# Kernel optimization log

Hardware: AMD Instinct MI355X
Metric: run time of the kernel (lower is better)

Reference implementation:

```python
import jax, jax.numpy as jnp
import numpy as np

BS, SEQ, D_IN, D_OUT = 4, 1024, 1024, 1024
N_SKILLS, RANK = 8, 4
SCALING = 1.0  # lora_alpha / rank, folded into one constant
NEG_INF = -1e38


def setup_inputs() -> dict:
    key = jax.random.key(0)
    ks = jax.random.split(key, 5)
    x = jax.random.normal(ks[0], (BS, SEQ, D_IN), jnp.float32)
    phi = jax.random.normal(ks[1], (D_IN, N_SKILLS), jnp.float32) * 0.02
    lora_a = jax.random.normal(ks[2], (N_SKILLS, D_IN, RANK), jnp.float32) * 0.02
    lora_b = jax.random.normal(ks[3], (N_SKILLS, RANK, D_OUT), jnp.float32) * 0.02
    W = jax.random.normal(ks[4], (D_OUT, D_IN), jnp.float32) * 0.02
    b = jnp.zeros((D_OUT,), jnp.float32)
    # left-padded sequences with an instruction prefix right after the padding
    pad_len = np.array([100, 0, 250, 50])
    inst_len = 300
    pad = np.zeros((BS, SEQ), np.int32)
    inst = np.zeros((BS, SEQ), np.int32)
    for i in range(BS):
        pad[i, pad_len[i]:] = 1
        inst[i, pad_len[i]:pad_len[i] + inst_len] = 1
    return {"x": x, "phi": phi, "lora_a": lora_a, "lora_b": lora_b,
            "W": W, "b": b,
            "inst_mask": jnp.asarray(inst), "pad_mask": jnp.asarray(pad)}


def _causal_prefix_mask(inst_mask, pad_mask):
    # faithful port of create_causal_prefix_mask (padding_side='left')
    bs, seq = inst_mask.shape
    first_one = jnp.argmax(inst_mask, axis=1, keepdims=True)          # [b,1]
    n_ones = jnp.sum(inst_mask, axis=1, keepdims=True)                # [b,1]
    thresh = first_one + n_ones                                       # last_one_idx + 1
    exp = jnp.broadcast_to(thresh, (bs, seq))                         # [b,s]
    inv = jnp.maximum(seq - exp - jnp.arange(seq)[None, :], 0)[:, ::-1]
    m = (exp + inv) * pad_mask                                        # [b,s]
    m3 = m[:, :, None] * pad_mask[:, None, :]                         # [b,s,s]
    ar = jnp.arange(seq)[None, None, :]
    return ar < m3                                                    # bool [b,s,s]


def reference(x, phi, lora_a, lora_b, W, b, inst_mask, pad_mask):
    # router: mixing logits per token per skill
    mw = jnp.einsum('bsd,dn->bsn', x, phi)                            # [b,s,k]
    cm = _causal_prefix_mask(inst_mask, pad_mask)                     # [b,s,s]
    padf = pad_mask.astype(x.dtype)
    # expand over attended positions p, mask, softmax over p
    logits = jnp.where(cm[..., None], mw[:, :, None, :], NEG_INF)     # [b,s,p,k]
    logits = jnp.transpose(logits, (0, 3, 1, 2))                      # [b,k,s,p]
    D = jax.nn.softmax(logits, axis=-1)
    D = D * padf[:, None, :, None]                                    # zero padded query rows
    # token mixing: contract over source tokens (last axis of D)
    input_mixed = jnp.einsum('bsd,bkps->bkpd', x, D)                  # [b,k,s,d]
    # per-skill LoRA (n_splits == 1, q squeezed)
    ar_r = jnp.einsum('bksd,kdr->bskr', input_mixed, lora_a)          # [b,s,k,r]
    ad = jnp.einsum('bskr,krd->bskd', ar_r, lora_b)                   # [b,s,k,d_out]
    # softmax-weighted combine over skills
    C = jax.nn.softmax(mw, axis=-1)
    adapter_out = jnp.einsum('bsk,bskd->bsd', C, ad) * SCALING
    base = jnp.einsum('bsd,od->bso', x, W) + b
    return base + adapter_out
```

## Files before the change

kernel.cpp:

```cpp
#include <hip/hip_runtime.h>
#include <hip/hip_bf16.h>
#include <cstdint>

#define SEQ   1024
#define DOUT  1024
#define KDIM  1024
#define MTOT  4096
#define WCROWS 1104

typedef __bf16 bf16x8 __attribute__((ext_vector_type(8)));
typedef float  f32x4  __attribute__((ext_vector_type(4)));

__device__ inline unsigned short f2bf(float f) {
  union { float f; unsigned u; } a; a.f = f;
  unsigned r = a.u + 0x7fff + ((a.u >> 16) & 1);
  return (unsigned short)(r >> 16);
}

__device__ inline void gl16(const void* g, void* l) {
  __builtin_amdgcn_global_load_lds((__attribute__((address_space(1))) void*)g,
                                   (__attribute__((address_space(3))) void*)l, 16, 0, 0);
}

__global__ __launch_bounds__(256) void k_prep(const float4* __restrict__ x, ushort4* __restrict__ xb,
                                              const float* __restrict__ W, const float* __restrict__ phi,
                                              const float* __restrict__ la, const float* __restrict__ lb,
                                              unsigned short* __restrict__ Wc,
                                              const int* __restrict__ inst, int* __restrict__ thr) {
  int blk = blockIdx.x, tid = threadIdx.x;
  if (blk < 4096) {
    int i = blk * 256 + tid;
    float4 v = x[i];
    ushort4 o; o.x = f2bf(v.x); o.y = f2bf(v.y); o.z = f2bf(v.z); o.w = f2bf(v.w);
    xb[i] = o;
  } else if (blk < 8512) {
    int i = (blk - 4096) * 256 + tid;
    int row = i >> 10, d = i & 1023;
    float v;
    if (row < 1024)       v = W[i];
    else if (row < 1032)  v = phi[d * 8 + (row - 1024)];
    else if (row < 1064)  { int kr = row - 1032; v = la[(kr >> 2) * 4096 + d * 4 + (kr & 3)]; }
    else if (row < 1072)  v = 0.f;
    else                  v = lb[(row - 1072) * 1024 + d];
    Wc[i] = f2bf(v);
  } else {
    int b = tid >> 6, lane = tid & 63;
    int fo = 1 << 30, no = 0;
#pragma unroll
    for (int j = 0; j < 16; ++j) {
      int p = j * 64 + lane;
      int iv = inst[b * SEQ + p];
      if (iv > 0) fo = min(fo, p);
      no += iv;
    }
#pragma unroll
    for (int d = 1; d < 64; d <<= 1) { fo = min(fo, __shfl_xor(fo, d)); no += __shfl_xor(no, d); }
    if (lane == 0) thr[b] = (no > 0) ? fo + no : 0;
  }
}

__global__ __launch_bounds__(256) void k_mwz(const unsigned short* __restrict__ xb,
                                             const unsigned short* __restrict__ Wc,
                                             float* __restrict__ mwzP) {
  __shared__ unsigned short As[64 * 32];
  __shared__ unsigned short Bs[48 * 32];
  int bm = blockIdx.x, ks = blockIdx.y;
  int t = threadIdx.x, wave = t >> 6, lane = t & 63;
  int quad = lane >> 4, lr = lane & 15;
  f32x4 acc[3];
#pragma unroll
  for (int i = 0; i < 3; ++i) acc[i] = (f32x4){0.f, 0.f, 0.f, 0.f};
  const unsigned short* aG = xb + (size_t)bm * 64 * KDIM + ks * 256;
  const unsigned short* bG = Wc + (size_t)1024 * KDIM + ks * 256;
  int r0 = t >> 2, c0 = (t & 3) * 8;
  for (int kb = 0; kb < 256; kb += 32) {
    __syncthreads();
    gl16(aG + (size_t)r0 * KDIM + kb + c0, &As[wave * 512]);
    if (t < 192) gl16(bG + (size_t)r0 * KDIM + kb + c0, &Bs[wave * 512]);
    __syncthreads();
    bf16x8 af = *(const bf16x8*)&As[(wave * 16 + lr) * 32 + quad * 8];
#pragma unroll
    for (int ni = 0; ni < 3; ++ni) {
      bf16x8 bfr = *(const bf16x8*)&Bs[(ni * 16 + lr) * 32 + quad * 8];
      acc[ni] = __builtin_amdgcn_mfma_f32_16x16x32_bf16(af, bfr, acc[ni], 0, 0, 0);
    }
  }
#pragma unroll
  for (int ni = 0; ni < 3; ++ni) {
    int c = ni * 16 + lr;
#pragma unroll
    for (int rg = 0; rg < 4; ++rg) {
      int row = bm * 64 + wave * 16 + quad * 4 + rg;
      if (c < 40) mwzP[(size_t)(ks * 40 + c) * MTOT + row] = acc[ni][rg];
    }
  }
}

__global__ __launch_bounds__(1024) void k_scan_gate(const float* __restrict__ mwzP,
                                                    const int* __restrict__ pad, const int* __restrict__ thr,
                                                    unsigned short* __restrict__ gb) {
  int b = blockIdx.x, c = blockIdx.y;
  int tid = threadIdx.x, wv = tid >> 6, lane = tid & 63;
  __shared__ float wsz[16], wsp[16];
  __shared__ float sv, spc;
  int q = b * SEQ + tid;
  float pm = (float)pad[q];
  float z = 0.f;
#pragma unroll
  for (int s = 0; s < 4; ++s) z += mwzP[(size_t)(s * 40 + 8 + c) * MTOT + q];
  z *= pm;
  float vz = z, vp = pm;
#pragma unroll
  for (int d = 1; d < 64; d <<= 1) {
    float oz = __shfl_up(vz, d), op = __shfl_up(vp, d);
    if (lane >= d) { vz += oz; vp += op; }
  }
  if (lane == 63) { wsz[wv] = vz; wsp[wv] = vp; }
  __syncthreads();
  if (wv == 0 && lane < 16) {
    float oz = wsz[lane], op = wsp[lane], sz = oz, sp = op;
#pragma unroll
    for (int d = 1; d < 16; d <<= 1) {
      float tz = __shfl_up(sz, d), tp = __shfl_up(sp, d);
      if (lane >= d) { sz += tz; sp += tp; }
    }
    wsz[lane] = sz - oz; wsp[lane] = sp - op;
  }
  __syncthreads();
  vz += wsz[wv]; vp += wsp[wv];
  int th = thr[b];
  if (th > 0 && tid == th - 1) { sv = vz; spc = vp; }
  __syncthreads();
  unsigned short o = 0;
  if (pm != 0.f) {
    bool own = (tid + 1 >= th);
    float Tv  = own ? vz : sv;
    float cnt = own ? vp : spc;
    float C[8], mx = -1e30f;
#pragma unroll
    for (int k = 0; k < 8; ++k) {
      float m = 0.f;
#pragma unroll
      for (int s = 0; s < 4; ++s) m += mwzP[(size_t)(s * 40 + k) * MTOT + q];
      C[k] = m; mx = fmaxf(mx, m);
    }
    float sm = 0.f;
#pragma unroll
    for (int k = 0; k < 8; ++k) { C[k] = __expf(C[k] - mx); sm += C[k]; }
    o = f2bf(C[c >> 2] * Tv / (sm * cnt));
  }
  gb[(size_t)q * 32 + c] = o;
}

__global__ __launch_bounds__(256) void k_gemm(const unsigned short* __restrict__ A,
                                              const unsigned short* __restrict__ Wc,
                                              const unsigned short* __restrict__ gb,
                                              float* __restrict__ out,
                                              const float* __restrict__ bias) {
  __shared__ unsigned short As[128 * 32];
  __shared__ unsigned short Bs[64 * 32];
  int bm = blockIdx.x, bn = blockIdx.y;
  int t = threadIdx.x;
  int wave = t >> 6, lane = t & 63;
  int wr = wave >> 1, wc = wave & 1;
  int quad = lane >> 4, lr = lane & 15;
  f32x4 acc[4][2];
#pragma unroll
  for (int i = 0; i < 4; i++)
#pragma unroll
    for (int j = 0; j < 2; j++) acc[i][j] = (f32x4){0.f, 0.f, 0.f, 0.f};

  const unsigned short* aG = A + (size_t)bm * 128 * KDIM;
  const unsigned short* bG = Wc + (size_t)bn * 64 * KDIM;
  int r0 = t >> 2, c0 = (t & 3) * 8;

  for (int kb = 0; kb < KDIM; kb += 32) {
    __syncthreads();
    gl16(aG + (size_t)r0 * KDIM + kb + c0, &As[wave * 512]);
    gl16(aG + (size_t)(r0 + 64) * KDIM + kb + c0, &As[2048 + wave * 512]);
    gl16(bG + (size_t)r0 * KDIM + kb + c0, &Bs[wave * 512]);
    __syncthreads();
    bf16x8 af[4], bfr[2];
#pragma unroll
    for (int mi = 0; mi < 4; mi++) af[mi]  = *(const bf16x8*)&As[(wr * 64 + mi * 16 + lr) * 32 + quad * 8];
#pragma unroll
    for (int ni = 0; ni < 2; ni++) bfr[ni] = *(const bf16x8*)&Bs[(wc * 32 + ni * 16 + lr) * 32 + quad * 8];
#pragma unroll
    for (int mi = 0; mi < 4; mi++)
#pragma unroll
      for (int ni = 0; ni < 2; ni++)
        acc[mi][ni] = __builtin_amdgcn_mfma_f32_16x16x32_bf16(af[mi], bfr[ni], acc[mi][ni], 0, 0, 0);
  }

  __syncthreads();
  gl16(gb + (size_t)(bm * 128 + r0) * 32 + c0,        &As[wave * 512]);
  gl16(gb + (size_t)(bm * 128 + 64 + r0) * 32 + c0,   &As[2048 + wave * 512]);
  {
    int kr = t >> 3, co = (t & 7) * 8;
    uint4 v = *(const uint4*)(Wc + (size_t)(1072 + kr) * KDIM + bn * 64 + co);
    *(uint4*)&Bs[kr * 64 + co] = v;
  }
  __syncthreads();
  bf16x8 af2[4];
#pragma unroll
  for (int mi = 0; mi < 4; mi++) af2[mi] = *(const bf16x8*)&As[(wr * 64 + mi * 16 + lr) * 32 + quad * 8];
#pragma unroll
  for (int ni = 0; ni < 2; ni++) {
    union { bf16x8 v; unsigned short u[8]; } bu;
    int col = wc * 32 + ni * 16 + lr;
#pragma unroll
    for (int j = 0; j < 8; ++j) bu.u[j] = Bs[(quad * 8 + j) * 64 + col];
#pragma unroll
    for (int mi = 0; mi < 4; mi++)
      acc[mi][ni] = __builtin_amdgcn_mfma_f32_16x16x32_bf16(af2[mi], bu.v, acc[mi][ni], 0, 0, 0);
  }

#pragma unroll
  for (int mi = 0; mi < 4; mi++) {
#pragma unroll
    for (int ni = 0; ni < 2; ni++) {
      int col = bn * 64 + wc * 32 + ni * 16 + lr;
      float bv = bias[col];
#pragma unroll
      for (int rg = 0; rg < 4; ++rg) {
        int row = bm * 128 + wr * 64 + mi * 16 + quad * 4 + rg;
        out[(size_t)row * DOUT + col] = acc[mi][ni][rg] + bv;
      }
    }
  }
}

extern "C" void kernel_launch(void* const* d_in, const int* in_sizes, int n_in,
                              void* d_out, int out_size, void* d_ws, size_t ws_size,
                              hipStream_t stream) {
  const float* x    = (const float*)d_in[0];
  const float* phi  = (const float*)d_in[1];
  const float* la   = (const float*)d_in[2];
  const float* lb   = (const float*)d_in[3];
  const float* W    = (const float*)d_in[4];
  const float* bias = (const float*)d_in[5];
  const int*   inst = (const int*)d_in[6];
  const int*   pad  = (const int*)d_in[7];
  float* out = (float*)d_out;

  char* ws = (char*)d_ws;
  unsigned short* xb  = (unsigned short*)ws;
  unsigned short* Wc  = (unsigned short*)(ws + 8388608);
  float* mwzP = (float*)(ws + 10649600);
  unsigned short* gb = (unsigned short*)(ws + 13271040);
  int*   thr  = (int*)(ws + 13533184);

  hipLaunchKernelGGL(k_prep,      dim3(8513),   dim3(256),  0, stream,
                     (const float4*)x, (ushort4*)xb, W, phi, la, lb, Wc, inst, thr);
  hipLaunchKernelGGL(k_mwz,       dim3(64, 4),  dim3(256),  0, stream, xb, Wc, mwzP);
  hipLaunchKernelGGL(k_scan_gate, dim3(4, 32),  dim3(1024), 0, stream, mwzP, pad, thr, gb);
  hipLaunchKernelGGL(k_gemm,      dim3(32, 16), dim3(256),  0, stream, xb, Wc, gb, out, bias);
}
```

Before: 116.7 us.

## Double-buffer LDS in GEMM kernels and pre-transpose LoRA B for tail stage

```diff
diff --git a/kernel.cpp b/kernel.cpp
--- a/kernel.cpp
+++ b/kernel.cpp
@@ -6,7 +6,7 @@
 #define DOUT  1024
 #define KDIM  1024
 #define MTOT  4096
-#define WCROWS 1104
+#define WCROWS 1072
 
 typedef __bf16 bf16x8 __attribute__((ext_vector_type(8)));
 typedef float  f32x4  __attribute__((ext_vector_type(4)));
@@ -25,7 +25,7 @@
 __global__ __launch_bounds__(256) void k_prep(const float4* __restrict__ x, ushort4* __restrict__ xb,
                                               const float* __restrict__ W, const float* __restrict__ phi,
                                               const float* __restrict__ la, const float* __restrict__ lb,
-                                              unsigned short* __restrict__ Wc,
+                                              unsigned short* __restrict__ Wc, unsigned short* __restrict__ B2T,
                                               const int* __restrict__ inst, int* __restrict__ thr) {
   int blk = blockIdx.x, tid = threadIdx.x;
   if (blk < 4096) {
@@ -33,16 +33,19 @@
     float4 v = x[i];
     ushort4 o; o.x = f2bf(v.x); o.y = f2bf(v.y); o.z = f2bf(v.z); o.w = f2bf(v.w);
     xb[i] = o;
-  } else if (blk < 8512) {
+  } else if (blk < 8384) {
     int i = (blk - 4096) * 256 + tid;
     int row = i >> 10, d = i & 1023;
     float v;
     if (row < 1024)       v = W[i];
     else if (row < 1032)  v = phi[d * 8 + (row - 1024)];
     else if (row < 1064)  { int kr = row - 1032; v = la[(kr >> 2) * 4096 + d * 4 + (kr & 3)]; }
-    else if (row < 1072)  v = 0.f;
-    else                  v = lb[(row - 1072) * 1024 + d];
+    else                  v = 0.f;
     Wc[i] = f2bf(v);
+  } else if (blk < 8512) {
+    int i = (blk - 8384) * 256 + tid;
+    int n = i >> 5, kr = i & 31;
+    B2T[i] = f2bf(lb[kr * 1024 + n]);
   } else {
     int b = tid >> 6, lane = tid & 63;
     int fo = 1 << 30, no = 0;
@@ -62,8 +65,8 @@
 __global__ __launch_bounds__(256) void k_mwz(const unsigned short* __restrict__ xb,
                                              const unsigned short* __restrict__ Wc,
                                              float* __restrict__ mwzP) {
-  __shared__ unsigned short As[64 * 32];
-  __shared__ unsigned short Bs[48 * 32];
+  __shared__ unsigned short As[2][64 * 32];
+  __shared__ unsigned short Bs[2][48 * 32];
   int bm = blockIdx.x, ks = blockIdx.y;
   int t = threadIdx.x, wave = t >> 6, lane = t & 63;
   int quad = lane >> 4, lr = lane & 15;
@@ -73,15 +76,20 @@
   const unsigned short* aG = xb + (size_t)bm * 64 * KDIM + ks * 256;
   const unsigned short* bG = Wc + (size_t)1024 * KDIM + ks * 256;
   int r0 = t >> 2, c0 = (t & 3) * 8;
-  for (int kb = 0; kb < 256; kb += 32) {
+
+#define MWZ_STAGE(i) { int buf_ = (i) & 1; int kb_ = (i) * 32;                         \
+    gl16(aG + (size_t)r0 * KDIM + kb_ + c0, &As[buf_][wave * 512]);                    \
+    if (wave < 3) gl16(bG + (size_t)r0 * KDIM + kb_ + c0, &Bs[buf_][wave * 512]); }
+
+  MWZ_STAGE(0)
+  for (int i = 0; i < 8; ++i) {
     __syncthreads();
-    gl16(aG + (size_t)r0 * KDIM + kb + c0, &As[wave * 512]);
-    if (t < 192) gl16(bG + (size_t)r0 * KDIM + kb + c0, &Bs[wave * 512]);
-    __syncthreads();
-    bf16x8 af = *(const bf16x8*)&As[(wave * 16 + lr) * 32 + quad * 8];
+    if (i < 7) MWZ_STAGE(i + 1)
+    int buf = i & 1;
+    bf16x8 af = *(const bf16x8*)&As[buf][(wave * 16 + lr) * 32 + quad * 8];
 #pragma unroll
     for (int ni = 0; ni < 3; ++ni) {
-      bf16x8 bfr = *(const bf16x8*)&Bs[(ni * 16 + lr) * 32 + quad * 8];
+      bf16x8 bfr = *(const bf16x8*)&Bs[buf][(ni * 16 + lr) * 32 + quad * 8];
       acc[ni] = __builtin_amdgcn_mfma_f32_16x16x32_bf16(af, bfr, acc[ni], 0, 0, 0);
     }
   }
@@ -155,10 +163,11 @@
 __global__ __launch_bounds__(256) void k_gemm(const unsigned short* __restrict__ A,
                                               const unsigned short* __restrict__ Wc,
                                               const unsigned short* __restrict__ gb,
+                                              const unsigned short* __restrict__ B2T,
                                               float* __restrict__ out,
                                               const float* __restrict__ bias) {
-  __shared__ unsigned short As[128 * 32];
-  __shared__ unsigned short Bs[64 * 32];
+  __shared__ unsigned short As[2][128 * 32];
+  __shared__ unsigned short Bs[2][64 * 32];
   int bm = blockIdx.x, bn = blockIdx.y;
   int t = threadIdx.x;
   int wave = t >> 6, lane = t & 63;
@@ -172,47 +181,36 @@
 
   const unsigned short* aG = A + (size_t)bm * 128 * KDIM;
   const unsigned short* bG = Wc + (size_t)bn * 64 * KDIM;
+  const unsigned short* gA = gb + (size_t)bm * 128 * 32;
+  const unsigned short* gB = B2T + (size_t)bn * 64 * 32;
   int r0 = t >> 2, c0 = (t & 3) * 8;
 
-  for (int kb = 0; kb < KDIM; kb += 32) {
+#define GEMM_STAGE(i) { int buf_ = (i) & 1;                                            \
+    if ((i) < 32) { int kb_ = (i) * 32;                                                \
+      gl16(aG + (size_t)r0 * KDIM + kb_ + c0,        &As[buf_][wave * 512]);           \
+      gl16(aG + (size_t)(r0 + 64) * KDIM + kb_ + c0, &As[buf_][2048 + wave * 512]);    \
+      gl16(bG + (size_t)r0 * KDIM + kb_ + c0,        &Bs[buf_][wave * 512]);           \
+    } else {                                                                           \
+      gl16(gA + (size_t)r0 * 32 + c0,        &As[buf_][wave * 512]);                   \
+      gl16(gA + (size_t)(r0 + 64) * 32 + c0, &As[buf_][2048 + wave * 512]);            \
+      gl16(gB + (size_t)r0 * 32 + c0,        &Bs[buf_][wave * 512]);                   \
+    } }
+
+  GEMM_STAGE(0)
+  for (int i = 0; i < 33; ++i) {
     __syncthreads();
-    gl16(aG + (size_t)r0 * KDIM + kb + c0, &As[wave * 512]);
-    gl16(aG + (size_t)(r0 + 64) * KDIM + kb + c0, &As[2048 + wave * 512]);
-    gl16(bG + (size_t)r0 * KDIM + kb + c0, &Bs[wave * 512]);
-    __syncthreads();
+    if (i < 32) GEMM_STAGE(i + 1)
+    int buf = i & 1;
     bf16x8 af[4], bfr[2];
 #pragma unroll
-    for (int mi = 0; mi < 4; mi++) af[mi]  = *(const bf16x8*)&As[(wr * 64 + mi * 16 + lr) * 32 + quad * 8];
-#pragma unroll
-    for (int ni = 0; ni < 2; ni++) bfr[ni] = *(const bf16x8*)&Bs[(wc * 32 + ni * 16 + lr) * 32 + quad * 8];
+    for (int mi = 0; mi < 4; mi++) af[mi]  = *(const bf16x8*)&As[buf][(wr * 64 + mi * 16 + lr) * 32 + quad * 8];
+#pragma unroll
+    for (int ni = 0; ni < 2; ni++) bfr[ni] = *(const bf16x8*)&Bs[buf][(wc * 32 + ni * 16 + lr) * 32 + quad * 8];
 #pragma unroll
     for (int mi = 0; mi < 4; mi++)
 #pragma unroll
       for (int ni = 0; ni < 2; ni++)
         acc[mi][ni] = __builtin_amdgcn_mfma_f32_16x16x32_bf16(af[mi], bfr[ni], acc[mi][ni], 0, 0, 0);
-  }
-
-  __syncthreads();
-  gl16(gb + (size_t)(bm * 128 + r0) * 32 + c0,        &As[wave * 512]);
-  gl16(gb + (size_t)(bm * 128 + 64 + r0) * 32 + c0,   &As[2048 + wave * 512]);
-  {
-    int kr = t >> 3, co = (t & 7) * 8;
-    uint4 v = *(const uint4*)(Wc + (size_t)(1072 + kr) * KDIM + bn * 64 + co);
-    *(uint4*)&Bs[kr * 64 + co] = v;
-  }
-  __syncthreads();
-  bf16x8 af2[4];
-#pragma unroll
-  for (int mi = 0; mi < 4; mi++) af2[mi] = *(const bf16x8*)&As[(wr * 64 + mi * 16 + lr) * 32 + quad * 8];
-#pragma unroll
-  for (int ni = 0; ni < 2; ni++) {
-    union { bf16x8 v; unsigned short u[8]; } bu;
-    int col = wc * 32 + ni * 16 + lr;
-#pragma unroll
-    for (int j = 0; j < 8; ++j) bu.u[j] = Bs[(quad * 8 + j) * 64 + col];
-#pragma unroll
-    for (int mi = 0; mi < 4; mi++)
-      acc[mi][ni] = __builtin_amdgcn_mfma_f32_16x16x32_bf16(af2[mi], bu.v, acc[mi][ni], 0, 0, 0);
   }
 
 #pragma unroll
@@ -246,13 +244,14 @@
   char* ws = (char*)d_ws;
   unsigned short* xb  = (unsigned short*)ws;
   unsigned short* Wc  = (unsigned short*)(ws + 8388608);
+  unsigned short* B2T = (unsigned short*)(ws + 10584064);
   float* mwzP = (float*)(ws + 10649600);
-  unsigned short* gb = (unsigned short*)(ws + 13271040);
+  unsigned short* gb  = (unsigned short*)(ws + 13271040);
   int*   thr  = (int*)(ws + 13533184);
 
   hipLaunchKernelGGL(k_prep,      dim3(8513),   dim3(256),  0, stream,
-                     (const float4*)x, (ushort4*)xb, W, phi, la, lb, Wc, inst, thr);
+                     (const float4*)x, (ushort4*)xb, W, phi, la, lb, Wc, B2T, inst, thr);
   hipLaunchKernelGGL(k_mwz,       dim3(64, 4),  dim3(256),  0, stream, xb, Wc, mwzP);
   hipLaunchKernelGGL(k_scan_gate, dim3(4, 32),  dim3(1024), 0, stream, mwzP, pad, thr, gb);
-  hipLaunchKernelGGL(k_gemm,      dim3(32, 16), dim3(256),  0, stream, xb, Wc, gb, out, bias);
-}
+  hipLaunchKernelGGL(k_gemm,      dim3(32, 16), dim3(256),  0, stream, xb, Wc, gb, B2T, out, bias);
+}
```

After: 119.9 us. 2.8% more time.

## Fuse prep into router GEMM and scan kernels, fold LoRA-B into main K loop

Applied to the files above, without the earlier changes.

```diff
diff --git a/kernel.cpp b/kernel.cpp
--- a/kernel.cpp
+++ b/kernel.cpp
@@ -6,7 +6,6 @@
 #define DOUT  1024
 #define KDIM  1024
 #define MTOT  4096
-#define WCROWS 1104
 
 typedef __bf16 bf16x8 __attribute__((ext_vector_type(8)));
 typedef float  f32x4  __attribute__((ext_vector_type(4)));
@@ -22,67 +21,53 @@
                                    (__attribute__((address_space(3))) void*)l, 16, 0, 0);
 }
 
-__global__ __launch_bounds__(256) void k_prep(const float4* __restrict__ x, ushort4* __restrict__ xb,
-                                              const float* __restrict__ W, const float* __restrict__ phi,
-                                              const float* __restrict__ la, const float* __restrict__ lb,
-                                              unsigned short* __restrict__ Wc,
-                                              const int* __restrict__ inst, int* __restrict__ thr) {
-  int blk = blockIdx.x, tid = threadIdx.x;
-  if (blk < 4096) {
-    int i = blk * 256 + tid;
-    float4 v = x[i];
+__global__ __launch_bounds__(256) void k_mwz(const float* __restrict__ x, unsigned short* __restrict__ xb,
+                                             const float* __restrict__ phi, const float* __restrict__ la,
+                                             float* __restrict__ mwzP) {
+  __shared__ __align__(16) unsigned short Bs[48 * 264];
+  int bm = blockIdx.x, ks = blockIdx.y;
+  int tid = threadIdx.x, wave = tid >> 6, lane = tid & 63;
+  int quad = lane >> 4, lr = lane & 15;
+
+#pragma unroll
+  for (int j = 0; j < 16; ++j) {
+    int u = j * 256 + tid;
+    int row = u >> 6, c4 = u & 63;
+    size_t base = (size_t)(bm * 64 + row) * KDIM + ks * 256;
+    float4 v = *((const float4*)(x + base) + c4);
     ushort4 o; o.x = f2bf(v.x); o.y = f2bf(v.y); o.z = f2bf(v.z); o.w = f2bf(v.w);
-    xb[i] = o;
-  } else if (blk < 8512) {
-    int i = (blk - 4096) * 256 + tid;
-    int row = i >> 10, d = i & 1023;
+    *((ushort4*)(xb + base) + c4) = o;
+  }
+  for (int e = tid; e < 48 * 256; e += 256) {
+    int r = e >> 8, c = e & 255, d = ks * 256 + c;
     float v;
-    if (row < 1024)       v = W[i];
-    else if (row < 1032)  v = phi[d * 8 + (row - 1024)];
-    else if (row < 1064)  { int kr = row - 1032; v = la[(kr >> 2) * 4096 + d * 4 + (kr & 3)]; }
-    else if (row < 1072)  v = 0.f;
-    else                  v = lb[(row - 1072) * 1024 + d];
-    Wc[i] = f2bf(v);
-  } else {
-    int b = tid >> 6, lane = tid & 63;
-    int fo = 1 << 30, no = 0;
-#pragma unroll
-    for (int j = 0; j < 16; ++j) {
-      int p = j * 64 + lane;
-      int iv = inst[b * SEQ + p];
-      if (iv > 0) fo = min(fo, p);
-      no += iv;
-    }
-#pragma unroll
-    for (int d = 1; d < 64; d <<= 1) { fo = min(fo, __shfl_xor(fo, d)); no += __shfl_xor(no, d); }
-    if (lane == 0) thr[b] = (no > 0) ? fo + no : 0;
-  }
-}
-
-__global__ __launch_bounds__(256) void k_mwz(const unsigned short* __restrict__ xb,
-                                             const unsigned short* __restrict__ Wc,
-                                             float* __restrict__ mwzP) {
-  __shared__ unsigned short As[64 * 32];
-  __shared__ unsigned short Bs[48 * 32];
-  int bm = blockIdx.x, ks = blockIdx.y;
-  int t = threadIdx.x, wave = t >> 6, lane = t & 63;
-  int quad = lane >> 4, lr = lane & 15;
+    if (r < 8)       v = phi[d * 8 + r];
+    else if (r < 40) { int kr = r - 8; v = la[(kr >> 2) * 4096 + d * 4 + (kr & 3)]; }
+    else             v = 0.f;
+    Bs[r * 264 + c] = f2bf(v);
+  }
+  int arow = bm * 64 + wave * 16 + lr;
+  const float* xr = x + (size_t)arow * KDIM + ks * 256 + quad * 8;
+  bf16x8 afr[8];
+#pragma unroll
+  for (int i = 0; i < 8; ++i) {
+    float4 a = *(const float4*)(xr + i * 32);
+    float4 b = *(const float4*)(xr + i * 32 + 4);
+    union { bf16x8 v; unsigned short u[8]; } t;
+    t.u[0] = f2bf(a.x); t.u[1] = f2bf(a.y); t.u[2] = f2bf(a.z); t.u[3] = f2bf(a.w);
+    t.u[4] = f2bf(b.x); t.u[5] = f2bf(b.y); t.u[6] = f2bf(b.z); t.u[7] = f2bf(b.w);
+    afr[i] = t.v;
+  }
+  __syncthreads();
   f32x4 acc[3];
 #pragma unroll
   for (int i = 0; i < 3; ++i) acc[i] = (f32x4){0.f, 0.f, 0.f, 0.f};
-  const unsigned short* aG = xb + (size_t)bm * 64 * KDIM + ks * 256;
-  const unsigned short* bG = Wc + (size_t)1024 * KDIM + ks * 256;
-  int r0 = t >> 2, c0 = (t & 3) * 8;
-  for (int kb = 0; kb < 256; kb += 32) {
-    __syncthreads();
-    gl16(aG + (size_t)r0 * KDIM + kb + c0, &As[wave * 512]);
-    if (t < 192) gl16(bG + (size_t)r0 * KDIM + kb + c0, &Bs[wave * 512]);
-    __syncthreads();
-    bf16x8 af = *(const bf16x8*)&As[(wave * 16 + lr) * 32 + quad * 8];
+  for (int i = 0; i < 8; ++i) {
+    int kb = i * 32;
 #pragma unroll
     for (int ni = 0; ni < 3; ++ni) {
-      bf16x8 bfr = *(const bf16x8*)&Bs[(ni * 16 + lr) * 32 + quad * 8];
-      acc[ni] = __builtin_amdgcn_mfma_f32_16x16x32_bf16(af, bfr, acc[ni], 0, 0, 0);
+      bf16x8 bfr = *(const bf16x8*)&Bs[(ni * 16 + lr) * 264 + kb + quad * 8];
+      acc[ni] = __builtin_amdgcn_mfma_f32_16x16x32_bf16(afr[i], bfr, acc[ni], 0, 0, 0);
     }
   }
 #pragma unroll
@@ -96,13 +81,45 @@
   }
 }
 
-__global__ __launch_bounds__(1024) void k_scan_gate(const float* __restrict__ mwzP,
-                                                    const int* __restrict__ pad, const int* __restrict__ thr,
-                                                    unsigned short* __restrict__ gb) {
-  int b = blockIdx.x, c = blockIdx.y;
-  int tid = threadIdx.x, wv = tid >> 6, lane = tid & 63;
+__global__ __launch_bounds__(1024) void k_sgp(const float* __restrict__ mwzP,
+                                              const int* __restrict__ inst, const int* __restrict__ pad,
+                                              const float* __restrict__ W, const float* __restrict__ lb,
+                                              unsigned short* __restrict__ Wc, unsigned short* __restrict__ B2T,
+                                              unsigned short* __restrict__ gb) {
+  int blk = blockIdx.x, tid = threadIdx.x;
+  if (blk >= 128) {
+    if (blk < 192) {
+      size_t base = (size_t)(blk - 128) * 16384;
+#pragma unroll
+      for (int j = 0; j < 16; ++j) { size_t e = base + j * 1024 + tid; Wc[e] = f2bf(W[e]); }
+    } else {
+#pragma unroll
+      for (int j = 0; j < 32; ++j) {
+        int e = j * 1024 + tid;
+        B2T[e] = f2bf(lb[(e & 31) * 1024 + (e >> 5)]);
+      }
+    }
+    return;
+  }
+  int b = blk >> 5, c = blk & 31;
+  int wv = tid >> 6, lane = tid & 63;
   __shared__ float wsz[16], wsp[16];
   __shared__ float sv, spc;
+  __shared__ int fos[16], nos[16], ths;
+  {
+    int iv = inst[b * SEQ + tid];
+    int fo = iv ? tid : (1 << 30), no = iv;
+#pragma unroll
+    for (int d = 1; d < 64; d <<= 1) { fo = min(fo, __shfl_xor(fo, d)); no += __shfl_xor(no, d); }
+    if (lane == 0) { fos[wv] = fo; nos[wv] = no; }
+  }
+  __syncthreads();
+  if (tid == 0) {
+    int F = 1 << 30, N = 0;
+#pragma unroll
+    for (int i = 0; i < 16; ++i) { F = min(F, fos[i]); N += nos[i]; }
+    ths = (N > 0) ? F + N : 0;
+  }
   int q = b * SEQ + tid;
   float pm = (float)pad[q];
   float z = 0.f;
@@ -128,7 +145,7 @@
   }
   __syncthreads();
   vz += wsz[wv]; vp += wsp[wv];
-  int th = thr[b];
+  int th = ths;
   if (th > 0 && tid == th - 1) { sv = vz; spc = vp; }
   __syncthreads();
   unsigned short o = 0;
@@ -155,6 +172,7 @@
 __global__ __launch_bounds__(256) void k_gemm(const unsigned short* __restrict__ A,
                                               const unsigned short* __restrict__ Wc,
                                               const unsigned short* __restrict__ gb,
+                                              const unsigned short* __restrict__ B2T,
                                               float* __restrict__ out,
                                               const float* __restrict__ bias) {
   __shared__ unsigned short As[128 * 32];
@@ -172,13 +190,22 @@
 
   const unsigned short* aG = A + (size_t)bm * 128 * KDIM;
   const unsigned short* bG = Wc + (size_t)bn * 64 * KDIM;
+  const unsigned short* gA = gb + (size_t)bm * 128 * 32;
+  const unsigned short* gB = B2T + (size_t)bn * 64 * 32;
   int r0 = t >> 2, c0 = (t & 3) * 8;
 
-  for (int kb = 0; kb < KDIM; kb += 32) {
+  for (int i = 0; i < 33; ++i) {
     __syncthreads();
-    gl16(aG + (size_t)r0 * KDIM + kb + c0, &As[wave * 512]);
-    gl16(aG + (size_t)(r0 + 64) * KDIM + kb + c0, &As[2048 + wave * 512]);
-    gl16(bG + (size_t)r0 * KDIM + kb + c0, &Bs[wave * 512]);
+    if (i < 32) {
+      int kb = i * 32;
+      gl16(aG + (size_t)r0 * KDIM + kb + c0,        &As[wave * 512]);
+      gl16(aG + (size_t)(r0 + 64) * KDIM + kb + c0, &As[2048 + wave * 512]);
+      gl16(bG + (size_t)r0 * KDIM + kb + c0,        &Bs[wave * 512]);
+    } else {
+      gl16(gA + (size_t)r0 * 32 + c0,        &As[wave * 512]);
+      gl16(gA + (size_t)(r0 + 64) * 32 + c0, &As[2048 + wave * 512]);
+      gl16(gB + (size_t)r0 * 32 + c0,        &Bs[wave * 512]);
+    }
     __syncthreads();
     bf16x8 af[4], bfr[2];
 #pragma unroll
@@ -190,29 +217,6 @@
 #pragma unroll
       for (int ni = 0; ni < 2; ni++)
         acc[mi][ni] = __builtin_amdgcn_mfma_f32_16x16x32_bf16(af[mi], bfr[ni], acc[mi][ni], 0, 0, 0);
-  }
-
-  __syncthreads();
-  gl16(gb + (size_t)(bm * 128 + r0) * 32 + c0,        &As[wave * 512]);
-  gl16(gb + (size_t)(bm * 128 + 64 + r0) * 32 + c0,   &As[2048 + wave * 512]);
-  {
-    int kr = t >> 3, co = (t & 7) * 8;
-    uint4 v = *(const uint4*)(Wc + (size_t)(1072 + kr) * KDIM + bn * 64 + co);
-    *(uint4*)&Bs[kr * 64 + co] = v;
-  }
-  __syncthreads();
-  bf16x8 af2[4];
-#pragma unroll
-  for (int mi = 0; mi < 4; mi++) af2[mi] = *(const bf16x8*)&As[(wr * 64 + mi * 16 + lr) * 32 + quad * 8];
-#pragma unroll
-  for (int ni = 0; ni < 2; ni++) {
-    union { bf16x8 v; unsigned short u[8]; } bu;
-    int col = wc * 32 + ni * 16 + lr;
-#pragma unroll
-    for (int j = 0; j < 8; ++j) bu.u[j] = Bs[(quad * 8 + j) * 64 + col];
-#pragma unroll
-    for (int mi = 0; mi < 4; mi++)
-      acc[mi][ni] = __builtin_amdgcn_mfma_f32_16x16x32_bf16(af2[mi], bu.v, acc[mi][ni], 0, 0, 0);
   }
 
 #pragma unroll
@@ -246,13 +250,11 @@
   char* ws = (char*)d_ws;
   unsigned short* xb  = (unsigned short*)ws;
   unsigned short* Wc  = (unsigned short*)(ws + 8388608);
-  float* mwzP = (float*)(ws + 10649600);
-  unsigned short* gb = (unsigned short*)(ws + 13271040);
-  int*   thr  = (int*)(ws + 13533184);
-
-  hipLaunchKernelGGL(k_prep,      dim3(8513),   dim3(256),  0, stream,
-                     (const float4*)x, (ushort4*)xb, W, phi, la, lb, Wc, inst, thr);
-  hipLaunchKernelGGL(k_mwz,       dim3(64, 4),  dim3(256),  0, stream, xb, Wc, mwzP);
-  hipLaunchKernelGGL(k_scan_gate, dim3(4, 32),  dim3(1024), 0, stream, mwzP, pad, thr, gb);
-  hipLaunchKernelGGL(k_gemm,      dim3(32, 16), dim3(256),  0, stream, xb, Wc, gb, out, bias);
-}
+  unsigned short* B2T = (unsigned short*)(ws + 10485760);
+  float* mwzP = (float*)(ws + 10551296);
+  unsigned short* gb  = (unsigned short*)(ws + 13172736);
+
+  hipLaunchKernelGGL(k_mwz,  dim3(64, 4),  dim3(256),  0, stream, x, xb, phi, la, mwzP);
+  hipLaunchKernelGGL(k_sgp,  dim3(193),    dim3(1024), 0, stream, mwzP, inst, pad, W, lb, Wc, B2T, gb);
+  hipLaunchKernelGGL(k_gemm, dim3(32, 16), dim3(256),  0, stream, xb, Wc, gb, B2T, out, bias);
+}
```

Result: slower. 131.5 us (+12.7%).
